# Kernel optimization log

Measured on AMD Instinct MI355X. Metric: run time of the kernel, lower is better.

Reference implementation:

```python
import jax, jax.numpy as jnp
import numpy as np

SQRT_D = 32  # ceil(sqrt(d_out)) with d_out = 1024
D_OUT = 1024


def setup_inputs() -> dict:
    key = jax.random.key(0)
    k1, k2, k3 = jax.random.split(key, 3)
    x = jax.random.normal(k1, (8, 4096, 1024), dtype=jnp.float32)
    scale = 1.0 / np.sqrt(SQRT_D)
    L = jax.random.normal(k2, (SQRT_D, SQRT_D, SQRT_D), dtype=jnp.float32) * scale
    R = jax.random.normal(k3, (SQRT_D, SQRT_D, SQRT_D), dtype=jnp.float32) * scale
    return {"x": x, "L": L, "R": R}


def reference(x, L, R):
    # MonarchOutProjection with proj_type == 'Monarch' (d_in*n_heads == d_out,
    # hd == sqrt_d**2 so no padding). Monarch: permute -> blockdiag(L) ->
    # permute -> blockdiag(R) -> permute, then slice to d_out.
    b, n, hd = x.shape
    s = SQRT_D
    # rearrange '... (m n) -> ... (n m)': view (m, n) then transpose.
    h = x.reshape(b, n, s, s)          # (..., m, n_inner)
    h = jnp.swapaxes(h, -1, -2)        # (..., block, inner)
    # blockdiag_matmul with L: einsum 'bnm,...bm->...bn'
    h = jnp.einsum('bnm,...bm->...bn', L, h)
    # rearrange '... (m n) -> ... (n m)' on the flattened result == transpose
    h = jnp.swapaxes(h, -1, -2)
    # blockdiag_matmul with R
    h = jnp.einsum('bnm,...bm->...bn', R, h)
    # final rearrange '... (m n) -> ... (n m)'
    h = jnp.swapaxes(h, -1, -2)
    out = h.reshape(b, n, hd)
    return out[..., :D_OUT]
```

## Files before the change

### kernel.cpp

```cpp
#include <hip/hip_runtime.h>
#include <hip/hip_bf16.h>


typedef __attribute__((ext_vector_type(8))) short short8;
typedef __attribute__((ext_vector_type(4))) float floatx4;

__device__ __forceinline__ unsigned int pack2bf(float a, float b) {
    __hip_bfloat162 h = __float22bfloat162_rn(float2{a, b});
    return *(unsigned int*)&h;
}

__device__ __forceinline__ void block_sync() {
    asm volatile("s_waitcnt lgkmcnt(0)" ::: "memory");
    __builtin_amdgcn_s_barrier();
    asm volatile("" ::: "memory");
}

__global__ void prep_weights(const float* __restrict__ L, const float* __restrict__ R,
                             unsigned short* __restrict__ Lb, unsigned short* __restrict__ Rb) {
    const int t = blockIdx.x * 256 + threadIdx.x;
    const float* src        = (t < 4096) ? L : R;
    unsigned short* dst     = (t < 4096) ? Lb : Rb;
    const int i    = t & 4095;
    const int lane = i & 63;
    const int pq   = i >> 6;
    const int p    = pq >> 1;
    const int qt   = pq & 1;
    const int q    = qt * 16 + (lane & 15);
    const int m0   = (lane >> 4) * 8;
    const float* s = src + (p * 32 + q) * 32 + m0;
    uint4 o;
    o.x = pack2bf(s[0], s[1]);
    o.y = pack2bf(s[2], s[3]);
    o.z = pack2bf(s[4], s[5]);
    o.w = pack2bf(s[6], s[7]);
    *(uint4*)(dst + (size_t)i * 8) = o;
}

__global__ __launch_bounds__(256, 3)
void monarch_kernel(const float* __restrict__ x,
                    const unsigned short* __restrict__ Lb,
                    const unsigned short* __restrict__ Rb,
                    float* __restrict__ out) {
    __shared__ __align__(16) unsigned short buf[16][1024];

    const int tid  = threadIdx.x;
    const int w    = tid >> 6;
    const int lane = tid & 63;
    const int tl   = lane & 15;
    const int quad = lane >> 4;
    const int c    = tid * 4;
    const long tok0 = (long)blockIdx.x * 16;

    float4 xv[16];
    #pragma unroll
    for (int t = 0; t < 16; ++t)
        xv[t] = *(const float4*)(x + (tok0 + t) * 1024 + c);

    short8 la[8][2];
    #pragma unroll
    for (int pp = 0; pp < 8; ++pp) {
        const int p = w * 8 + pp;
        la[pp][0] = *(const short8*)(Lb + (size_t)((p * 2 + 0) * 64 + lane) * 8);
        la[pp][1] = *(const short8*)(Lb + (size_t)((p * 2 + 1) * 64 + lane) * 8);
    }

    #pragma unroll
    for (int t = 0; t < 16; ++t) {
        const unsigned long long v =
            ((unsigned long long)pack2bf(xv[t].z, xv[t].w) << 32) | pack2bf(xv[t].x, xv[t].y);
        *(unsigned long long*)&buf[t][c ^ (t << 2)] = v;
    }
    block_sync();

    short8 b1[8];
    #pragma unroll
    for (int pp = 0; pp < 8; ++pp) {
        const int p = w * 8 + pp;
        #pragma unroll
        for (int j = 0; j < 8; ++j)
            b1[pp][j] = (short)buf[tl][(quad * 256 + j * 32 + p) ^ (tl << 2)];
    }
    block_sync();

    #pragma unroll
    for (int pp = 0; pp < 8; ++pp) {
        const int p = w * 8 + pp;
        #pragma unroll
        for (int qt = 0; qt < 2; ++qt) {
            floatx4 acc = {0.f, 0.f, 0.f, 0.f};
            acc = __builtin_amdgcn_mfma_f32_16x16x32_bf16(la[pp][qt], b1[pp], acc, 0, 0, 0);
            const unsigned long long v =
                ((unsigned long long)pack2bf(acc[2], acc[3]) << 32) | pack2bf(acc[0], acc[1]);
            const int el = p * 32 + qt * 16 + quad * 4;
            *(unsigned long long*)&buf[tl][el ^ (tl << 2)] = v;
        }
    }

    short8 ra[8][2];
    #pragma unroll
    for (int qq = 0; qq < 8; ++qq) {
        const int q = w * 8 + qq;
        ra[qq][0] = *(const short8*)(Rb + (size_t)((q * 2 + 0) * 64 + lane) * 8);
        ra[qq][1] = *(const short8*)(Rb + (size_t)((q * 2 + 1) * 64 + lane) * 8);
    }
    block_sync();

    short8 b2[8];
    #pragma unroll
    for (int qq = 0; qq < 8; ++qq) {
        const int q = w * 8 + qq;
        #pragma unroll
        for (int j = 0; j < 8; ++j)
            b2[qq][j] = (short)buf[tl][((quad * 8 + j) * 32 + q) ^ (tl << 2)];
    }
    block_sync();

    #pragma unroll
    for (int qq = 0; qq < 8; ++qq) {
        const int q = w * 8 + qq;
        #pragma unroll
        for (int rt = 0; rt < 2; ++rt) {
            floatx4 z = {0.f, 0.f, 0.f, 0.f};
            const floatx4 acc =
                __builtin_amdgcn_mfma_f32_16x16x32_bf16(ra[qq][rt], b2[qq], z, 0, 0, 0);
            const unsigned int lo = pack2bf(acc[0], acc[1]);
            const unsigned int hi = pack2bf(acc[2], acc[3]);
            const int r0 = rt * 16 + quad * 4;
            buf[tl][((r0    ) * 32 + q) ^ (tl << 2)] = (unsigned short)lo;
            buf[tl][((r0 + 1) * 32 + q) ^ (tl << 2)] = (unsigned short)(lo >> 16);
            buf[tl][((r0 + 2) * 32 + q) ^ (tl << 2)] = (unsigned short)hi;
            buf[tl][((r0 + 3) * 32 + q) ^ (tl << 2)] = (unsigned short)(hi >> 16);
        }
    }
    block_sync();

    #pragma unroll
    for (int t = 0; t < 16; ++t) {
        const unsigned long long v = *(const unsigned long long*)&buf[t][c ^ (t << 2)];
        const unsigned int lo = (unsigned int)v;
        const unsigned int hi = (unsigned int)(v >> 32);
        float4 o;
        o.x = __uint_as_float(lo << 16);
        o.y = __uint_as_float(lo & 0xffff0000u);
        o.z = __uint_as_float(hi << 16);
        o.w = __uint_as_float(hi & 0xffff0000u);
        *(float4*)(out + (tok0 + t) * 1024 + c) = o;
    }
}

extern "C" void kernel_launch(void* const* d_in, const int* in_sizes, int n_in,
                              void* d_out, int out_size, void* d_ws, size_t ws_size,
                              hipStream_t stream) {
    const float* x = (const float*)d_in[0];
    const float* L = (const float*)d_in[1];
    const float* R = (const float*)d_in[2];
    float* out = (float*)d_out;

    unsigned short* Lb = (unsigned short*)d_ws;
    unsigned short* Rb = Lb + 32768;

    prep_weights<<<32, 256, 0, stream>>>(L, R, Lb, Rb);

    const int n_tokens = 8 * 4096;
    const int grid = n_tokens / 16;
    monarch_kernel<<<grid, 256, 0, stream>>>(x, Lb, Rb, out);
}
```

Before: 243.4 us.

## Load x directly into MFMA operand layout and pad LDS instead of XOR swizzle

Each thread now loads x in the exact pattern needed for the first MFMA operand, with the operands swapped, so the first LDS round trip and two barriers go away. The intermediate buffers use padded strides (PS/QS/TS) in place of the XOR swizzle, and the second MFMA results are held in registers across a barrier before being scattered to LDS. The x global loads become 32-byte chunks with a stride of 128 bytes per thread, which may coalesce worse than the old contiguous float4 loads, and the extra live registers could put pressure on occupancy.

```diff
diff --git a/kernel.cpp b/kernel.cpp
--- a/kernel.cpp
+++ b/kernel.cpp
@@ -5,9 +5,16 @@
 typedef __attribute__((ext_vector_type(8))) short short8;
 typedef __attribute__((ext_vector_type(4))) float floatx4;
 
+#define PS 18
+#define QS 584
+#define TS 1028
+
 __device__ __forceinline__ unsigned int pack2bf(float a, float b) {
     __hip_bfloat162 h = __float22bfloat162_rn(float2{a, b});
     return *(unsigned int*)&h;
+}
+__device__ __forceinline__ float bf2f(unsigned int u16) {
+    return __uint_as_float(u16 << 16);
 }
 
 __device__ __forceinline__ void block_sync() {
@@ -42,46 +49,41 @@
                     const unsigned short* __restrict__ Lb,
                     const unsigned short* __restrict__ Rb,
                     float* __restrict__ out) {
-    __shared__ __align__(16) unsigned short buf[16][1024];
+    __shared__ __align__(16) unsigned short lds[18688];
 
     const int tid  = threadIdx.x;
     const int w    = tid >> 6;
     const int lane = tid & 63;
     const int tl   = lane & 15;
     const int quad = lane >> 4;
-    const int c    = tid * 4;
     const long tok0 = (long)blockIdx.x * 16;
 
-    float4 xv[16];
+    const float* xb = x + (tok0 + tl) * 1024 + w * 8;
+    float4 xa[8], xc[8];
     #pragma unroll
-    for (int t = 0; t < 16; ++t)
-        xv[t] = *(const float4*)(x + (tok0 + t) * 1024 + c);
+    for (int j = 0; j < 8; ++j) {
+        xa[j] = *(const float4*)(xb + (quad * 8 + j) * 32);
+        xc[j] = *(const float4*)(xb + (quad * 8 + j) * 32 + 4);
+    }
 
-    short8 la[8][2];
+    short8 a1[8];
+    #pragma unroll
+    for (int pp = 0; pp < 8; ++pp) {
+        #pragma unroll
+        for (int r = 0; r < 4; ++r) {
+            const float lo = (pp < 4) ? xa[2 * r    ][pp] : xc[2 * r    ][pp - 4];
+            const float hi = (pp < 4) ? xa[2 * r + 1][pp] : xc[2 * r + 1][pp - 4];
+            ((unsigned int*)&a1[pp])[r] = pack2bf(lo, hi);
+        }
+    }
+
+    short8 lb[8][2];
     #pragma unroll
     for (int pp = 0; pp < 8; ++pp) {
         const int p = w * 8 + pp;
-        la[pp][0] = *(const short8*)(Lb + (size_t)((p * 2 + 0) * 64 + lane) * 8);
-        la[pp][1] = *(const short8*)(Lb + (size_t)((p * 2 + 1) * 64 + lane) * 8);
+        lb[pp][0] = *(const short8*)(Lb + (size_t)((p * 2 + 0) * 64 + lane) * 8);
+        lb[pp][1] = *(const short8*)(Lb + (size_t)((p * 2 + 1) * 64 + lane) * 8);
     }
-
-    #pragma unroll
-    for (int t = 0; t < 16; ++t) {
-        const unsigned long long v =
-            ((unsigned long long)pack2bf(xv[t].z, xv[t].w) << 32) | pack2bf(xv[t].x, xv[t].y);
-        *(unsigned long long*)&buf[t][c ^ (t << 2)] = v;
-    }
-    block_sync();
-
-    short8 b1[8];
-    #pragma unroll
-    for (int pp = 0; pp < 8; ++pp) {
-        const int p = w * 8 + pp;
-        #pragma unroll
-        for (int j = 0; j < 8; ++j)
-            b1[pp][j] = (short)buf[tl][(quad * 256 + j * 32 + p) ^ (tl << 2)];
-    }
-    block_sync();
 
     #pragma unroll
     for (int pp = 0; pp < 8; ++pp) {
@@ -89,11 +91,10 @@
         #pragma unroll
         for (int qt = 0; qt < 2; ++qt) {
             floatx4 acc = {0.f, 0.f, 0.f, 0.f};
-            acc = __builtin_amdgcn_mfma_f32_16x16x32_bf16(la[pp][qt], b1[pp], acc, 0, 0, 0);
-            const unsigned long long v =
-                ((unsigned long long)pack2bf(acc[2], acc[3]) << 32) | pack2bf(acc[0], acc[1]);
-            const int el = p * 32 + qt * 16 + quad * 4;
-            *(unsigned long long*)&buf[tl][el ^ (tl << 2)] = v;
+            acc = __builtin_amdgcn_mfma_f32_16x16x32_bf16(a1[pp], lb[pp][qt], acc, 0, 0, 0);
+            const int el = (qt * 16 + tl) * QS + p * PS + quad * 4;
+            *(unsigned int*)&lds[el]     = pack2bf(acc[0], acc[1]);
+            *(unsigned int*)&lds[el + 2] = pack2bf(acc[2], acc[3]);
         }
     }
 
@@ -106,13 +107,22 @@
     }
     block_sync();
 
-    short8 b2[8];
+    unsigned long long y2p[8][2];
     #pragma unroll
     for (int qq = 0; qq < 8; ++qq) {
         const int q = w * 8 + qq;
+        short8 b2;
         #pragma unroll
         for (int j = 0; j < 8; ++j)
-            b2[qq][j] = (short)buf[tl][((quad * 8 + j) * 32 + q) ^ (tl << 2)];
+            b2[j] = (short)lds[q * QS + (quad * 8 + j) * PS + tl];
+        #pragma unroll
+        for (int rt = 0; rt < 2; ++rt) {
+            floatx4 z = {0.f, 0.f, 0.f, 0.f};
+            const floatx4 acc =
+                __builtin_amdgcn_mfma_f32_16x16x32_bf16(ra[qq][rt], b2, z, 0, 0, 0);
+            y2p[qq][rt] = ((unsigned long long)pack2bf(acc[2], acc[3]) << 32)
+                        | pack2bf(acc[0], acc[1]);
+        }
     }
     block_sync();
 
@@ -121,30 +131,25 @@
         const int q = w * 8 + qq;
         #pragma unroll
         for (int rt = 0; rt < 2; ++rt) {
-            floatx4 z = {0.f, 0.f, 0.f, 0.f};
-            const floatx4 acc =
-                __builtin_amdgcn_mfma_f32_16x16x32_bf16(ra[qq][rt], b2[qq], z, 0, 0, 0);
-            const unsigned int lo = pack2bf(acc[0], acc[1]);
-            const unsigned int hi = pack2bf(acc[2], acc[3]);
-            const int r0 = rt * 16 + quad * 4;
-            buf[tl][((r0    ) * 32 + q) ^ (tl << 2)] = (unsigned short)lo;
-            buf[tl][((r0 + 1) * 32 + q) ^ (tl << 2)] = (unsigned short)(lo >> 16);
-            buf[tl][((r0 + 2) * 32 + q) ^ (tl << 2)] = (unsigned short)hi;
-            buf[tl][((r0 + 3) * 32 + q) ^ (tl << 2)] = (unsigned short)(hi >> 16);
+            const unsigned long long v = y2p[qq][rt];
+            #pragma unroll
+            for (int rr = 0; rr < 4; ++rr) {
+                const int r = rt * 16 + quad * 4 + rr;
+                lds[tl * TS + r * 32 + q] = (unsigned short)(v >> (16 * rr));
+            }
         }
     }
     block_sync();
 
+    const int c = tid * 4;
     #pragma unroll
     for (int t = 0; t < 16; ++t) {
-        const unsigned long long v = *(const unsigned long long*)&buf[t][c ^ (t << 2)];
+        const unsigned long long v = *(const unsigned long long*)&lds[t * TS + c];
         const unsigned int lo = (unsigned int)v;
         const unsigned int hi = (unsigned int)(v >> 32);
         float4 o;
-        o.x = __uint_as_float(lo << 16);
-        o.y = __uint_as_float(lo & 0xffff0000u);
-        o.z = __uint_as_float(hi << 16);
-        o.w = __uint_as_float(hi & 0xffff0000u);
+        o.x = bf2f(lo & 0xffffu); o.y = bf2f(lo >> 16);
+        o.z = bf2f(hi & 0xffffu); o.w = bf2f(hi >> 16);
         *(float4*)(out + (tok0 + t) * 1024 + c) = o;
     }
 }
```

Result: slower. 249.5 us (+2.5%).
